# Optimization experiments

Hardware: AMD Instinct MI355X
Metric: run time of the kernel (lower is better)

Reference implementation:

```python
import jax, jax.numpy as jnp
import numpy as np

ALPHA = 5.0  # spatial bandwidth
BETA = 5.0   # feature (bilateral) bandwidth
EPS = 1e-20


def gauss_filter(features, values):
    """Exact dense Gaussian (bilateral) filter: the math the permutohedral
    lattice (pl.apply) approximates.
    features: [B, D, N], values: [B, C, N] -> [B, C, N]
    Q[b,c,i] = sum_j exp(-0.5*||f_i - f_j||^2) * v[b,c,j]
    """
    sq = jnp.sum(features * features, axis=1)  # [B, N]
    d2 = sq[:, :, None] + sq[:, None, :] - 2.0 * jnp.einsum('bdi,bdj->bij', features, features)
    K = jnp.exp(-0.5 * jnp.maximum(d2, 0.0))  # [B, N, N]
    return jnp.einsum('bij,bcj->bci', K, values)


def setup_inputs() -> dict:
    key = jax.random.key(0)
    k1, k2 = jax.random.split(key)
    I = jax.random.normal(k1, (2, 3, 18, 18, 18), dtype=jnp.float32)
    U = jax.random.normal(k2, (2, 4, 18, 18, 18), dtype=jnp.float32)
    return {"I": I, "U": U}


def reference(I, U):
    B, n_feat, X, Y, Z = I.shape
    N = X * Y * Z
    n_ch = U.shape[1]
    # spatial coordinates, scaled by alpha (smoothness kernel part)
    gx, gy, gz = jnp.meshgrid(jnp.arange(X), jnp.arange(Y), jnp.arange(Z), indexing='ij')
    coords = jnp.stack([gx, gy, gz], 0).astype(I.dtype)            # [3, X, Y, Z]
    coords = jnp.broadcast_to(coords[None], (B, 3, X, Y, Z))
    feats = jnp.concatenate([coords / ALPHA, I / BETA], axis=1)    # [B, 3+n_feat, X, Y, Z]
    feats = feats.reshape(B, n_feat + 3, N)
    # normalization: filter an all-ones signal (use_norm=True path)
    ones = jnp.ones((B, 1, N), dtype=I.dtype)
    spatial_norm = 1.0 / jnp.sqrt(gauss_filter(feats, ones) + EPS)  # [B, 1, N]
    # unary -> softmax over channels
    Uf = U.reshape(B, n_ch, N)
    H1 = jax.nn.softmax(Uf, axis=1)                                 # [B, C, N]
    # pairwise message passing (normalized bilateral filter)
    Q1 = gauss_filter(feats, H1 * spatial_norm) * spatial_norm      # [B, C, N]
    # trace(Q1_flat.T @ (1 - H1_flat)) == elementwise sum (same reshape on both)
    loss = jnp.sum(Q1 * (1.0 - H1))
    return loss
```

## Files before the change

kernel.cpp:

```cpp
#include <hip/hip_runtime.h>

#define B_      2
#define NCH     4
#define DIMX    18
#define NPT     (18*18*18)
#define TIL     183
#define ITIL    184
#define NPTP    (ITIL*32)
#define IBLOCKS 23
#define JSP     16
#define NB      (IBLOCKS*JSP*B_)
#define FSC     (1.2011224087864498f / 5.0f)
#define QPAD    -30000.0f

typedef __attribute__((ext_vector_type(8)))  short short8;
typedef __attribute__((ext_vector_type(4)))  short short4_;
typedef __attribute__((ext_vector_type(16))) float f32x16;
typedef __attribute__((ext_vector_type(4)))  int   int4_;

#define EXP2(x) __builtin_amdgcn_exp2f(x)
#define MFMA32(a, b, c) __builtin_amdgcn_mfma_f32_32x32x16_bf16(a, b, c, 0, 0, 0)

__device__ __forceinline__ unsigned short bf16rtn(float f) {
  unsigned u = __float_as_uint(f);
  u += 0x7fffu + ((u >> 16) & 1u);
  return (unsigned short)(u >> 16);
}
__device__ __forceinline__ float bf2f(unsigned short s) {
  return __uint_as_float(((unsigned)s) << 16);
}

__device__ __forceinline__ float blockReduceSum(float v) {
  #pragma unroll
  for (int o = 32; o > 0; o >>= 1) v += __shfl_down(v, o, 64);
  __shared__ float red[4];
  int wid = threadIdx.x >> 6, lane = threadIdx.x & 63;
  if (lane == 0) red[wid] = v;
  __syncthreads();
  v = (threadIdx.x < 4) ? red[threadIdx.x] : 0.0f;
  if (wid == 0) {
    v += __shfl_down(v, 2, 64);
    v += __shfl_down(v, 1, 64);
  }
  return v;
}

__global__ void prep_kernel(const float* __restrict__ I, const float* __restrict__ U,
                            short8* __restrict__ AHI, short8* __restrict__ BHL,
                            float4* __restrict__ H) {
  const short8 zer = {0, 0, 0, 0, 0, 0, 0, 0};
  int idx = blockIdx.x * 256 + threadIdx.x;
  if (idx >= B_ * NPTP) return;
  int bb = idx / NPTP, n = idx - bb * NPTP;
  short8 ahi, bhi, blo;
  float4 hh;
  if (n < NPT) {
    int x = n / (DIMX * DIMX);
    int rem = n - x * DIMX * DIMX;
    int y = rem / DIMX, z = rem - y * DIMX;
    float f0 = x * FSC, f1 = y * FSC, f2 = z * FSC;
    float f3 = I[(size_t)(bb * 3 + 0) * NPT + n] * FSC;
    float f4 = I[(size_t)(bb * 3 + 1) * NPT + n] * FSC;
    float f5 = I[(size_t)(bb * 3 + 2) * NPT + n] * FSC;
    float q = -0.5f * (f0*f0 + f1*f1 + f2*f2 + f3*f3 + f4*f4 + f5*f5);
    float av[8] = {f0, f1, f2, f3, f4, f5, q, 1.0f};
    float bv[8] = {f0, f1, f2, f3, f4, f5, 1.0f, q};
    #pragma unroll
    for (int e = 0; e < 8; ++e) {
      ahi[e] = (short)bf16rtn(av[e]);
      unsigned short bh = bf16rtn(bv[e]);
      bhi[e] = (short)bh;
      blo[e] = (short)bf16rtn(bv[e] - bf2f(bh));
    }
    float u0 = U[(size_t)(bb * NCH + 0) * NPT + n];
    float u1 = U[(size_t)(bb * NCH + 1) * NPT + n];
    float u2 = U[(size_t)(bb * NCH + 2) * NPT + n];
    float u3 = U[(size_t)(bb * NCH + 3) * NPT + n];
    float m = fmaxf(fmaxf(u0, u1), fmaxf(u2, u3));
    float e0 = __expf(u0-m), e1 = __expf(u1-m), e2 = __expf(u2-m), e3 = __expf(u3-m);
    float inv = 1.0f / (e0 + e1 + e2 + e3);
    hh = make_float4(e0*inv, e1*inv, e2*inv, e3*inv);
  } else {
    ahi = zer; bhi = zer; blo = zer;
    bhi[7] = (short)bf16rtn(QPAD);
    hh = make_float4(0.f, 0.f, 0.f, 0.f);
  }
  AHI[idx] = ahi;
  BHL[(size_t)idx * 2]     = bhi;
  BHL[(size_t)idx * 2 + 1] = blo;
  H[idx] = hh;
}

__device__ __forceinline__ float expsum16(const f32x16 acc) {
  float e[16];
  #pragma unroll
  for (int r = 0; r < 16; ++r) e[r] = EXP2(acc[r]);
  float s8[8];
  #pragma unroll
  for (int r = 0; r < 8; ++r) s8[r] = e[2*r] + e[2*r+1];
  float s4[4];
  #pragma unroll
  for (int r = 0; r < 4; ++r) s4[r] = s8[2*r] + s8[2*r+1];
  return (s4[0] + s4[1]) + (s4[2] + s4[3]);
}

__global__ void __launch_bounds__(256) pass1_kernel(const short8* __restrict__ AHI,
                                                    const short8* __restrict__ BHL,
                                                    float* __restrict__ part) {
  const short8 zer = {0, 0, 0, 0, 0, 0, 0, 0};
  int tid = threadIdx.x, wid = tid >> 6, l = tid & 63, h = l >> 5, li = l & 31;
  int bb = blockIdx.z, jc = blockIdx.y;
  int i0 = (blockIdx.x * 8 + wid) * 32 + li;
  int i1 = i0 + 128;
  size_t pbase = (size_t)bb * NPTP;
  int t0 = jc * TIL / JSP, t1 = (jc + 1) * TIL / JSP;

  short8 b1_0 = AHI[pbase + i0];
  short8 b1_1 = AHI[pbase + i1];

  f32x16 z;
  #pragma unroll
  for (int r = 0; r < 16; ++r) z[r] = 0.0f;

  float sacc0 = 0.0f, sacc1 = 0.0f;
  short8 a_cur = BHL[(pbase + (size_t)t0 * 32 + li) * 2 + h];
  for (int t = t0; t < t1; ++t) {
    short8 a_nxt = (t + 1 < t1) ? BHL[(pbase + (size_t)(t+1) * 32 + li) * 2 + h] : zer;
    f32x16 acc0 = MFMA32(a_cur, b1_0, z);
    f32x16 acc1 = MFMA32(a_cur, b1_1, z);
    sacc0 += expsum16(acc0);
    sacc1 += expsum16(acc1);
    a_cur = a_nxt;
  }
  sacc0 += __shfl_xor(sacc0, 32, 64);
  sacc1 += __shfl_xor(sacc1, 32, 64);
  if (h == 0) {
    part[((size_t)bb * JSP + jc) * NPTP + i0] = sacc0;
    part[((size_t)bb * JSP + jc) * NPTP + i1] = sacc1;
  }
}

__global__ void finalize_kernel(const float4* __restrict__ H, const float* __restrict__ part,
                                unsigned short* __restrict__ Vt, float4* __restrict__ G4) {
  int idx = blockIdx.x * 256 + threadIdx.x;
  if (idx >= B_ * NPTP) return;
  int bb = idx / NPTP, ii = idx - bb * NPTP;
  if (ii < NPT) {
    float s = 0.0f;
    #pragma unroll
    for (int k = 0; k < JSP; ++k) s += part[((size_t)bb * JSP + k) * NPTP + ii];
    float nrm = rsqrtf(s + 1e-20f);
    float4 hh = H[idx];
    Vt[((size_t)bb * 4 + 0) * NPTP + ii] = bf16rtn(hh.x * nrm);
    Vt[((size_t)bb * 4 + 1) * NPTP + ii] = bf16rtn(hh.y * nrm);
    Vt[((size_t)bb * 4 + 2) * NPTP + ii] = bf16rtn(hh.z * nrm);
    Vt[((size_t)bb * 4 + 3) * NPTP + ii] = bf16rtn(hh.w * nrm);
    G4[idx] = make_float4((1.0f - hh.x) * nrm, (1.0f - hh.y) * nrm,
                          (1.0f - hh.z) * nrm, (1.0f - hh.w) * nrm);
  } else {
    Vt[((size_t)bb * 4 + 0) * NPTP + ii] = 0;
    Vt[((size_t)bb * 4 + 1) * NPTP + ii] = 0;
    Vt[((size_t)bb * 4 + 2) * NPTP + ii] = 0;
    Vt[((size_t)bb * 4 + 3) * NPTP + ii] = 0;
    G4[idx] = make_float4(0.f, 0.f, 0.f, 0.f);
  }
}

__device__ __forceinline__ void ldv(const unsigned short* __restrict__ vrow, int j32,
                                    int h, bool cok, short8* vf1, short8* vf2) {
  const short4_ zer4 = {0, 0, 0, 0};
  short4_ va = cok ? *(const short4_*)(vrow + j32 + 4*h)      : zer4;
  short4_ vb = cok ? *(const short4_*)(vrow + j32 + 8 + 4*h)  : zer4;
  short4_ vc = cok ? *(const short4_*)(vrow + j32 + 16 + 4*h) : zer4;
  short4_ vd = cok ? *(const short4_*)(vrow + j32 + 24 + 4*h) : zer4;
  short8 f1, f2;
  #pragma unroll
  for (int e = 0; e < 4; ++e) {
    f1[e] = va[e]; f1[4 + e] = vb[e];
    f2[e] = vc[e]; f2[4 + e] = vd[e];
  }
  *vf1 = f1; *vf2 = f2;
}

__device__ __forceinline__ void pv_tile(const f32x16 acc, const short8 vf1,
                                        const short8 vf2, f32x16* d2) {
  float w[16];
  #pragma unroll
  for (int r = 0; r < 16; ++r) w[r] = EXP2(acc[r]);
  int p[8];
  #pragma unroll
  for (int r = 0; r < 8; ++r)
    asm("v_cvt_pk_bf16_f32 %0, %1, %2" : "=v"(p[r]) : "v"(w[2*r]), "v"(w[2*r+1]));
  union { int4_ iv; short8 sv; } u1, u2;
  u1.iv = (int4_){p[0], p[1], p[2], p[3]};
  u2.iv = (int4_){p[4], p[5], p[6], p[7]};
  f32x16 d = *d2;
  d = MFMA32(vf1, u1.sv, d);
  d = MFMA32(vf2, u2.sv, d);
  *d2 = d;
}

__global__ void __launch_bounds__(256) pass2_kernel(const short8* __restrict__ AHI,
                                                    const short8* __restrict__ BHL,
                                                    const unsigned short* __restrict__ Vt,
                                                    const float4* __restrict__ G4,
                                                    float* __restrict__ pl) {
  const short8 zer = {0, 0, 0, 0, 0, 0, 0, 0};
  int tid = threadIdx.x, wid = tid >> 6, l = tid & 63, h = l >> 5, li = l & 31;
  int bb = blockIdx.z, jc = blockIdx.y;
  int i0 = (blockIdx.x * 8 + wid) * 32 + li;
  int i1 = i0 + 128;
  size_t pbase = (size_t)bb * NPTP;
  int t0 = jc * TIL / JSP, t1 = (jc + 1) * TIL / JSP;

  short8 b1_0 = AHI[pbase + i0];
  short8 b1_1 = AHI[pbase + i1];
  float4 g0 = G4[pbase + i0];
  float4 g1 = G4[pbase + i1];
  bool cok = li < 4;
  const unsigned short* vrow = Vt + ((size_t)bb * 4 + (cok ? li : 0)) * NPTP;

  f32x16 z;
  #pragma unroll
  for (int r = 0; r < 16; ++r) z[r] = 0.0f;

  f32x16 d2_0 = z, d2_1 = z;

  short8 a_cur = BHL[(pbase + (size_t)t0 * 32 + li) * 2 + h];
  short8 vf1c, vf2c;
  ldv(vrow, t0 * 32, h, cok, &vf1c, &vf2c);

  for (int t = t0; t < t1; ++t) {
    short8 a_nxt = zer, vf1n = zer, vf2n = zer;
    if (t + 1 < t1) {
      a_nxt = BHL[(pbase + (size_t)(t+1) * 32 + li) * 2 + h];
      ldv(vrow, (t + 1) * 32, h, cok, &vf1n, &vf2n);
    }
    f32x16 acc0 = MFMA32(a_cur, b1_0, z);
    f32x16 acc1 = MFMA32(a_cur, b1_1, z);
    pv_tile(acc0, vf1c, vf2c, &d2_0);
    pv_tile(acc1, vf1c, vf2c, &d2_1);
    a_cur = a_nxt; vf1c = vf1n; vf2c = vf2n;
  }

  float loss = d2_0[0] * g0.x + d2_0[1] * g0.y + d2_0[2] * g0.z + d2_0[3] * g0.w
             + d2_1[0] * g1.x + d2_1[1] * g1.y + d2_1[2] * g1.z + d2_1[3] * g1.w;
  float r = blockReduceSum(loss);
  if (tid == 0) pl[((size_t)bb * JSP + jc) * IBLOCKS + blockIdx.x] = r;
}

__global__ void reduce_kernel(const float* __restrict__ pl, int n, float* __restrict__ out) {
  float v = 0.0f;
  for (int k = threadIdx.x; k < n; k += 256) v += pl[k];
  float r = blockReduceSum(v);
  if (threadIdx.x == 0) out[0] = r;
}

extern "C" void kernel_launch(void* const* d_in, const int* in_sizes, int n_in,
                              void* d_out, int out_size, void* d_ws, size_t ws_size,
                              hipStream_t stream) {
  const float* I = (const float*)d_in[0];
  const float* U = (const float*)d_in[1];
  float* out = (float*)d_out;

  char* w = (char*)d_ws;
  short8* AHI = (short8*)w;                 w += (size_t)B_ * NPTP * 16;
  short8* BHL = (short8*)w;                 w += (size_t)B_ * NPTP * 32;
  float4* H   = (float4*)w;                 w += (size_t)B_ * NPTP * 16;
  float*  part = (float*)w;                 w += (size_t)B_ * JSP * NPTP * 4;
  unsigned short* Vt = (unsigned short*)w;  w += (size_t)B_ * 4 * NPTP * 2;
  float4* G4  = (float4*)w;                 w += (size_t)B_ * NPTP * 16;
  float*  pl  = (float*)w;                  w += (size_t)NB * 4;

  prep_kernel<<<(B_ * NPTP + 255) / 256, 256, 0, stream>>>(I, U, AHI, BHL, H);
  dim3 grid(IBLOCKS, JSP, B_);
  pass1_kernel<<<grid, 256, 0, stream>>>(AHI, BHL, part);
  finalize_kernel<<<(B_ * NPTP + 255) / 256, 256, 0, stream>>>(H, part, Vt, G4);
  pass2_kernel<<<grid, 256, 0, stream>>>(AHI, BHL, Vt, G4, pl);
  reduce_kernel<<<1, 256, 0, stream>>>(pl, NB, out);
}
```

Baseline: 42.45 us.

## Fuse prep, finalize and reduce into two pass kernels with LDS-staged features

Removes the separate prep, finalize and reduce kernels. Each pass block now computes its j-tile features (bf16 hi/lo) and normalized values directly into shared memory, and builds its i-side features on the fly. The final reduction happens in the last-arriving block, using an atomic counter reset by a memset. The j-split rises from 16 to 22 so the grid has more blocks, and launch bounds request 4 blocks per CU. This cuts launch count and global round-trips. The cost is redundant per-block feature, softmax and norm recomputation, and the norm now sums 22 partials instead of 16.

```diff
diff --git a/kernel.cpp b/kernel.cpp
--- a/kernel.cpp
+++ b/kernel.cpp
@@ -8,13 +8,13 @@
 #define ITIL    184
 #define NPTP    (ITIL*32)
 #define IBLOCKS 23
-#define JSP     16
+#define JSP     22
 #define NB      (IBLOCKS*JSP*B_)
+#define MAXT    9
 #define FSC     (1.2011224087864498f / 5.0f)
 #define QPAD    -30000.0f
 
 typedef __attribute__((ext_vector_type(8)))  short short8;
-typedef __attribute__((ext_vector_type(4)))  short short4_;
 typedef __attribute__((ext_vector_type(16))) float f32x16;
 typedef __attribute__((ext_vector_type(4)))  int   int4_;
 
@@ -42,53 +42,62 @@
     v += __shfl_down(v, 2, 64);
     v += __shfl_down(v, 1, 64);
   }
+  __syncthreads();
   return v;
 }
 
-__global__ void prep_kernel(const float* __restrict__ I, const float* __restrict__ U,
-                            short8* __restrict__ AHI, short8* __restrict__ BHL,
-                            float4* __restrict__ H) {
-  const short8 zer = {0, 0, 0, 0, 0, 0, 0, 0};
-  int idx = blockIdx.x * 256 + threadIdx.x;
-  if (idx >= B_ * NPTP) return;
-  int bb = idx / NPTP, n = idx - bb * NPTP;
-  short8 ahi, bhi, blo;
-  float4 hh;
+__device__ __forceinline__ void feat6(const float* __restrict__ I, int bb, int n,
+                                      float f[6], float* q) {
+  int x = n / (DIMX * DIMX);
+  int rem = n - x * DIMX * DIMX;
+  int y = rem / DIMX, zz = rem - y * DIMX;
+  f[0] = x * FSC; f[1] = y * FSC; f[2] = zz * FSC;
+  f[3] = I[(size_t)(bb * 3 + 0) * NPT + n] * FSC;
+  f[4] = I[(size_t)(bb * 3 + 1) * NPT + n] * FSC;
+  f[5] = I[(size_t)(bb * 3 + 2) * NPT + n] * FSC;
+  *q = -0.5f * (f[0]*f[0] + f[1]*f[1] + f[2]*f[2] + f[3]*f[3] + f[4]*f[4] + f[5]*f[5]);
+}
+
+__device__ __forceinline__ void bfeat(const float* __restrict__ I, int bb, int n,
+                                      short8* hi, short8* lo) {
+  short8 h_ = {0,0,0,0,0,0,0,0}, l_ = {0,0,0,0,0,0,0,0};
   if (n < NPT) {
-    int x = n / (DIMX * DIMX);
-    int rem = n - x * DIMX * DIMX;
-    int y = rem / DIMX, z = rem - y * DIMX;
-    float f0 = x * FSC, f1 = y * FSC, f2 = z * FSC;
-    float f3 = I[(size_t)(bb * 3 + 0) * NPT + n] * FSC;
-    float f4 = I[(size_t)(bb * 3 + 1) * NPT + n] * FSC;
-    float f5 = I[(size_t)(bb * 3 + 2) * NPT + n] * FSC;
-    float q = -0.5f * (f0*f0 + f1*f1 + f2*f2 + f3*f3 + f4*f4 + f5*f5);
-    float av[8] = {f0, f1, f2, f3, f4, f5, q, 1.0f};
-    float bv[8] = {f0, f1, f2, f3, f4, f5, 1.0f, q};
+    float f[6], q;
+    feat6(I, bb, n, f, &q);
+    float bv[8] = {f[0], f[1], f[2], f[3], f[4], f[5], 1.0f, q};
     #pragma unroll
     for (int e = 0; e < 8; ++e) {
-      ahi[e] = (short)bf16rtn(av[e]);
       unsigned short bh = bf16rtn(bv[e]);
-      bhi[e] = (short)bh;
-      blo[e] = (short)bf16rtn(bv[e] - bf2f(bh));
-    }
-    float u0 = U[(size_t)(bb * NCH + 0) * NPT + n];
-    float u1 = U[(size_t)(bb * NCH + 1) * NPT + n];
-    float u2 = U[(size_t)(bb * NCH + 2) * NPT + n];
-    float u3 = U[(size_t)(bb * NCH + 3) * NPT + n];
-    float m = fmaxf(fmaxf(u0, u1), fmaxf(u2, u3));
-    float e0 = __expf(u0-m), e1 = __expf(u1-m), e2 = __expf(u2-m), e3 = __expf(u3-m);
-    float inv = 1.0f / (e0 + e1 + e2 + e3);
-    hh = make_float4(e0*inv, e1*inv, e2*inv, e3*inv);
+      h_[e] = (short)bh;
+      l_[e] = (short)bf16rtn(bv[e] - bf2f(bh));
+    }
   } else {
-    ahi = zer; bhi = zer; blo = zer;
-    bhi[7] = (short)bf16rtn(QPAD);
-    hh = make_float4(0.f, 0.f, 0.f, 0.f);
-  }
-  AHI[idx] = ahi;
-  BHL[(size_t)idx * 2]     = bhi;
-  BHL[(size_t)idx * 2 + 1] = blo;
-  H[idx] = hh;
+    h_[7] = (short)bf16rtn(QPAD);
+  }
+  *hi = h_; *lo = l_;
+}
+
+__device__ __forceinline__ short8 afeat(const float* __restrict__ I, int bb, int n) {
+  short8 a = {0,0,0,0,0,0,0,0};
+  if (n < NPT) {
+    float f[6], q;
+    feat6(I, bb, n, f, &q);
+    float av[8] = {f[0], f[1], f[2], f[3], f[4], f[5], q, 1.0f};
+    #pragma unroll
+    for (int e = 0; e < 8; ++e) a[e] = (short)bf16rtn(av[e]);
+  }
+  return a;
+}
+
+__device__ __forceinline__ float4 softmax4(const float* __restrict__ U, int bb, int n) {
+  float u0 = U[(size_t)(bb * NCH + 0) * NPT + n];
+  float u1 = U[(size_t)(bb * NCH + 1) * NPT + n];
+  float u2 = U[(size_t)(bb * NCH + 2) * NPT + n];
+  float u3 = U[(size_t)(bb * NCH + 3) * NPT + n];
+  float m = fmaxf(fmaxf(u0, u1), fmaxf(u2, u3));
+  float e0 = __expf(u0-m), e1 = __expf(u1-m), e2 = __expf(u2-m), e3 = __expf(u3-m);
+  float inv = 1.0f / (e0 + e1 + e2 + e3);
+  return make_float4(e0*inv, e1*inv, e2*inv, e3*inv);
 }
 
 __device__ __forceinline__ float expsum16(const f32x16 acc) {
@@ -104,33 +113,38 @@
   return (s4[0] + s4[1]) + (s4[2] + s4[3]);
 }
 
-__global__ void __launch_bounds__(256) pass1_kernel(const short8* __restrict__ AHI,
-                                                    const short8* __restrict__ BHL,
-                                                    float* __restrict__ part) {
-  const short8 zer = {0, 0, 0, 0, 0, 0, 0, 0};
+__global__ void __launch_bounds__(256, 4) pass1_kernel(const float* __restrict__ I,
+                                                       float* __restrict__ part) {
+  __shared__ short8 bhl[MAXT * 32 * 2];
   int tid = threadIdx.x, wid = tid >> 6, l = tid & 63, h = l >> 5, li = l & 31;
-  int bb = blockIdx.z, jc = blockIdx.y;
-  int i0 = (blockIdx.x * 8 + wid) * 32 + li;
+  int bb = blockIdx.z, jc = blockIdx.y, ib = blockIdx.x;
+  int t0 = jc * TIL / JSP, t1 = (jc + 1) * TIL / JSP;
+  int cnt = (t1 - t0) * 32;
+
+  for (int p = tid; p < cnt; p += 256) {
+    short8 hi, lo;
+    bfeat(I, bb, t0 * 32 + p, &hi, &lo);
+    bhl[p * 2]     = hi;
+    bhl[p * 2 + 1] = lo;
+  }
+
+  int i0 = (ib * 8 + wid) * 32 + li;
   int i1 = i0 + 128;
-  size_t pbase = (size_t)bb * NPTP;
-  int t0 = jc * TIL / JSP, t1 = (jc + 1) * TIL / JSP;
-
-  short8 b1_0 = AHI[pbase + i0];
-  short8 b1_1 = AHI[pbase + i1];
+  short8 b1_0 = afeat(I, bb, i0);
+  short8 b1_1 = afeat(I, bb, i1);
+  __syncthreads();
 
   f32x16 z;
   #pragma unroll
   for (int r = 0; r < 16; ++r) z[r] = 0.0f;
 
   float sacc0 = 0.0f, sacc1 = 0.0f;
-  short8 a_cur = BHL[(pbase + (size_t)t0 * 32 + li) * 2 + h];
   for (int t = t0; t < t1; ++t) {
-    short8 a_nxt = (t + 1 < t1) ? BHL[(pbase + (size_t)(t+1) * 32 + li) * 2 + h] : zer;
-    f32x16 acc0 = MFMA32(a_cur, b1_0, z);
-    f32x16 acc1 = MFMA32(a_cur, b1_1, z);
+    short8 a = bhl[((t - t0) * 32 + li) * 2 + h];
+    f32x16 acc0 = MFMA32(a, b1_0, z);
+    f32x16 acc1 = MFMA32(a, b1_1, z);
     sacc0 += expsum16(acc0);
     sacc1 += expsum16(acc1);
-    a_cur = a_nxt;
   }
   sacc0 += __shfl_xor(sacc0, 32, 64);
   sacc1 += __shfl_xor(sacc1, 32, 64);
@@ -140,120 +154,130 @@
   }
 }
 
-__global__ void finalize_kernel(const float4* __restrict__ H, const float* __restrict__ part,
-                                unsigned short* __restrict__ Vt, float4* __restrict__ G4) {
-  int idx = blockIdx.x * 256 + threadIdx.x;
-  if (idx >= B_ * NPTP) return;
-  int bb = idx / NPTP, ii = idx - bb * NPTP;
-  if (ii < NPT) {
-    float s = 0.0f;
-    #pragma unroll
-    for (int k = 0; k < JSP; ++k) s += part[((size_t)bb * JSP + k) * NPTP + ii];
-    float nrm = rsqrtf(s + 1e-20f);
-    float4 hh = H[idx];
-    Vt[((size_t)bb * 4 + 0) * NPTP + ii] = bf16rtn(hh.x * nrm);
-    Vt[((size_t)bb * 4 + 1) * NPTP + ii] = bf16rtn(hh.y * nrm);
-    Vt[((size_t)bb * 4 + 2) * NPTP + ii] = bf16rtn(hh.z * nrm);
-    Vt[((size_t)bb * 4 + 3) * NPTP + ii] = bf16rtn(hh.w * nrm);
-    G4[idx] = make_float4((1.0f - hh.x) * nrm, (1.0f - hh.y) * nrm,
-                          (1.0f - hh.z) * nrm, (1.0f - hh.w) * nrm);
-  } else {
-    Vt[((size_t)bb * 4 + 0) * NPTP + ii] = 0;
-    Vt[((size_t)bb * 4 + 1) * NPTP + ii] = 0;
-    Vt[((size_t)bb * 4 + 2) * NPTP + ii] = 0;
-    Vt[((size_t)bb * 4 + 3) * NPTP + ii] = 0;
-    G4[idx] = make_float4(0.f, 0.f, 0.f, 0.f);
-  }
-}
-
-__device__ __forceinline__ void ldv(const unsigned short* __restrict__ vrow, int j32,
-                                    int h, bool cok, short8* vf1, short8* vf2) {
-  const short4_ zer4 = {0, 0, 0, 0};
-  short4_ va = cok ? *(const short4_*)(vrow + j32 + 4*h)      : zer4;
-  short4_ vb = cok ? *(const short4_*)(vrow + j32 + 8 + 4*h)  : zer4;
-  short4_ vc = cok ? *(const short4_*)(vrow + j32 + 16 + 4*h) : zer4;
-  short4_ vd = cok ? *(const short4_*)(vrow + j32 + 24 + 4*h) : zer4;
-  short8 f1, f2;
-  #pragma unroll
-  for (int e = 0; e < 4; ++e) {
-    f1[e] = va[e]; f1[4 + e] = vb[e];
-    f2[e] = vc[e]; f2[4 + e] = vd[e];
-  }
-  *vf1 = f1; *vf2 = f2;
-}
-
-__device__ __forceinline__ void pv_tile(const f32x16 acc, const short8 vf1,
-                                        const short8 vf2, f32x16* d2) {
-  float w[16];
-  #pragma unroll
-  for (int r = 0; r < 16; ++r) w[r] = EXP2(acc[r]);
-  int p[8];
-  #pragma unroll
-  for (int r = 0; r < 8; ++r)
-    asm("v_cvt_pk_bf16_f32 %0, %1, %2" : "=v"(p[r]) : "v"(w[2*r]), "v"(w[2*r+1]));
-  union { int4_ iv; short8 sv; } u1, u2;
-  u1.iv = (int4_){p[0], p[1], p[2], p[3]};
-  u2.iv = (int4_){p[4], p[5], p[6], p[7]};
-  f32x16 d = *d2;
-  d = MFMA32(vf1, u1.sv, d);
-  d = MFMA32(vf2, u2.sv, d);
-  *d2 = d;
-}
-
-__global__ void __launch_bounds__(256) pass2_kernel(const short8* __restrict__ AHI,
-                                                    const short8* __restrict__ BHL,
-                                                    const unsigned short* __restrict__ Vt,
-                                                    const float4* __restrict__ G4,
-                                                    float* __restrict__ pl) {
+__global__ void __launch_bounds__(256, 4) pass2_kernel(const float* __restrict__ I,
+                                                       const float* __restrict__ U,
+                                                       const float* __restrict__ part,
+                                                       float* __restrict__ pl,
+                                                       unsigned* __restrict__ cnt_,
+                                                       float* __restrict__ out) {
+  __shared__ short8 bhl[MAXT * 32 * 2];
+  __shared__ short8 vt8[MAXT * 4 * 4];
+  __shared__ bool isLast;
+  int tid = threadIdx.x, wid = tid >> 6, l = tid & 63, h = l >> 5, li = l & 31;
+  int bb = blockIdx.z, jc = blockIdx.y, ib = blockIdx.x;
+  int t0 = jc * TIL / JSP, t1 = (jc + 1) * TIL / JSP;
+  int cnt = (t1 - t0) * 32;
+  unsigned short* vtp = (unsigned short*)vt8;
+
+  for (int p = tid; p < cnt; p += 256) {
+    int j = t0 * 32 + p;
+    short8 hi, lo;
+    bfeat(I, bb, j, &hi, &lo);
+    bhl[p * 2]     = hi;
+    bhl[p * 2 + 1] = lo;
+    float4 hv = make_float4(0.f, 0.f, 0.f, 0.f);
+    float nrm = 0.0f;
+    if (j < NPT) {
+      float s = 0.0f;
+      #pragma unroll
+      for (int k = 0; k < JSP; ++k) s += part[((size_t)bb * JSP + k) * NPTP + j];
+      nrm = rsqrtf(s + 1e-20f);
+      hv = softmax4(U, bb, j);
+    }
+    int tt = p >> 5, jj = p & 31;
+    int g1 = jj >> 4, r = jj & 15;
+    int slot = (g1 * 2 + ((r >> 2) & 1)) * 8 + (r & 3) + 4 * (r >> 3);
+    vtp[(tt * 4 + 0) * 32 + slot] = bf16rtn(hv.x * nrm);
+    vtp[(tt * 4 + 1) * 32 + slot] = bf16rtn(hv.y * nrm);
+    vtp[(tt * 4 + 2) * 32 + slot] = bf16rtn(hv.z * nrm);
+    vtp[(tt * 4 + 3) * 32 + slot] = bf16rtn(hv.w * nrm);
+  }
+
+  int i0 = (ib * 8 + wid) * 32 + li;
+  int i1 = i0 + 128;
+  short8 b1_0 = afeat(I, bb, i0);
+  short8 b1_1 = afeat(I, bb, i1);
+  float4 g0 = make_float4(0.f, 0.f, 0.f, 0.f), g1v = g0;
+  {
+    if (i0 < NPT) {
+      float s = 0.0f;
+      #pragma unroll
+      for (int k = 0; k < JSP; ++k) s += part[((size_t)bb * JSP + k) * NPTP + i0];
+      float nrm = rsqrtf(s + 1e-20f);
+      float4 hh = softmax4(U, bb, i0);
+      g0 = make_float4((1.f-hh.x)*nrm, (1.f-hh.y)*nrm, (1.f-hh.z)*nrm, (1.f-hh.w)*nrm);
+    }
+    if (i1 < NPT) {
+      float s = 0.0f;
+      #pragma unroll
+      for (int k = 0; k < JSP; ++k) s += part[((size_t)bb * JSP + k) * NPTP + i1];
+      float nrm = rsqrtf(s + 1e-20f);
+      float4 hh = softmax4(U, bb, i1);
+      g1v = make_float4((1.f-hh.x)*nrm, (1.f-hh.y)*nrm, (1.f-hh.z)*nrm, (1.f-hh.w)*nrm);
+    }
+  }
+  __syncthreads();
+
   const short8 zer = {0, 0, 0, 0, 0, 0, 0, 0};
-  int tid = threadIdx.x, wid = tid >> 6, l = tid & 63, h = l >> 5, li = l & 31;
-  int bb = blockIdx.z, jc = blockIdx.y;
-  int i0 = (blockIdx.x * 8 + wid) * 32 + li;
-  int i1 = i0 + 128;
-  size_t pbase = (size_t)bb * NPTP;
-  int t0 = jc * TIL / JSP, t1 = (jc + 1) * TIL / JSP;
-
-  short8 b1_0 = AHI[pbase + i0];
-  short8 b1_1 = AHI[pbase + i1];
-  float4 g0 = G4[pbase + i0];
-  float4 g1 = G4[pbase + i1];
   bool cok = li < 4;
-  const unsigned short* vrow = Vt + ((size_t)bb * 4 + (cok ? li : 0)) * NPTP;
+  int cc = cok ? li : 0;
 
   f32x16 z;
   #pragma unroll
   for (int r = 0; r < 16; ++r) z[r] = 0.0f;
-
   f32x16 d2_0 = z, d2_1 = z;
 
-  short8 a_cur = BHL[(pbase + (size_t)t0 * 32 + li) * 2 + h];
-  short8 vf1c, vf2c;
-  ldv(vrow, t0 * 32, h, cok, &vf1c, &vf2c);
-
   for (int t = t0; t < t1; ++t) {
-    short8 a_nxt = zer, vf1n = zer, vf2n = zer;
-    if (t + 1 < t1) {
-      a_nxt = BHL[(pbase + (size_t)(t+1) * 32 + li) * 2 + h];
-      ldv(vrow, (t + 1) * 32, h, cok, &vf1n, &vf2n);
-    }
-    f32x16 acc0 = MFMA32(a_cur, b1_0, z);
-    f32x16 acc1 = MFMA32(a_cur, b1_1, z);
-    pv_tile(acc0, vf1c, vf2c, &d2_0);
-    pv_tile(acc1, vf1c, vf2c, &d2_1);
-    a_cur = a_nxt; vf1c = vf1n; vf2c = vf2n;
+    int tt = t - t0;
+    short8 a = bhl[(tt * 32 + li) * 2 + h];
+    short8 vf1 = vt8[(tt * 4 + cc) * 4 + h];
+    short8 vf2 = vt8[(tt * 4 + cc) * 4 + 2 + h];
+    vf1 = cok ? vf1 : zer;
+    vf2 = cok ? vf2 : zer;
+
+    f32x16 acc0 = MFMA32(a, b1_0, z);
+    f32x16 acc1 = MFMA32(a, b1_1, z);
+
+    float w0[16], w1[16];
+    #pragma unroll
+    for (int r = 0; r < 16; ++r) { w0[r] = EXP2(acc0[r]); w1[r] = EXP2(acc1[r]); }
+    int p0[8], p1[8];
+    #pragma unroll
+    for (int r = 0; r < 8; ++r) {
+      asm("v_cvt_pk_bf16_f32 %0, %1, %2" : "=v"(p0[r]) : "v"(w0[2*r]), "v"(w0[2*r+1]));
+      asm("v_cvt_pk_bf16_f32 %0, %1, %2" : "=v"(p1[r]) : "v"(w1[2*r]), "v"(w1[2*r+1]));
+    }
+    union { int4_ iv; short8 sv; } u1a, u2a, u1b, u2b;
+    u1a.iv = (int4_){p0[0], p0[1], p0[2], p0[3]};
+    u2a.iv = (int4_){p0[4], p0[5], p0[6], p0[7]};
+    u1b.iv = (int4_){p1[0], p1[1], p1[2], p1[3]};
+    u2b.iv = (int4_){p1[4], p1[5], p1[6], p1[7]};
+
+    d2_0 = MFMA32(vf1, u1a.sv, d2_0);
+    d2_0 = MFMA32(vf2, u2a.sv, d2_0);
+    d2_1 = MFMA32(vf1, u1b.sv, d2_1);
+    d2_1 = MFMA32(vf2, u2b.sv, d2_1);
   }
 
   float loss = d2_0[0] * g0.x + d2_0[1] * g0.y + d2_0[2] * g0.z + d2_0[3] * g0.w
-             + d2_1[0] * g1.x + d2_1[1] * g1.y + d2_1[2] * g1.z + d2_1[3] * g1.w;
+             + d2_1[0] * g1v.x + d2_1[1] * g1v.y + d2_1[2] * g1v.z + d2_1[3] * g1v.w;
   float r = blockReduceSum(loss);
-  if (tid == 0) pl[((size_t)bb * JSP + jc) * IBLOCKS + blockIdx.x] = r;
-}
-
-__global__ void reduce_kernel(const float* __restrict__ pl, int n, float* __restrict__ out) {
-  float v = 0.0f;
-  for (int k = threadIdx.x; k < n; k += 256) v += pl[k];
-  float r = blockReduceSum(v);
-  if (threadIdx.x == 0) out[0] = r;
+
+  int blkflat = ((bb * JSP + jc) * IBLOCKS + ib);
+  if (tid == 0) {
+    pl[blkflat] = r;
+    __threadfence();
+    unsigned prev = atomicAdd(cnt_, 1u);
+    isLast = (prev == NB - 1);
+  }
+  __syncthreads();
+  if (isLast) {
+    __threadfence();
+    float v = 0.0f;
+    for (int k = tid; k < NB; k += 256) v += pl[k];
+    float rr = blockReduceSum(v);
+    if (tid == 0) out[0] = rr;
+  }
 }
 
 extern "C" void kernel_launch(void* const* d_in, const int* in_sizes, int n_in,
@@ -264,18 +288,12 @@
   float* out = (float*)d_out;
 
   char* w = (char*)d_ws;
-  short8* AHI = (short8*)w;                 w += (size_t)B_ * NPTP * 16;
-  short8* BHL = (short8*)w;                 w += (size_t)B_ * NPTP * 32;
-  float4* H   = (float4*)w;                 w += (size_t)B_ * NPTP * 16;
-  float*  part = (float*)w;                 w += (size_t)B_ * JSP * NPTP * 4;
-  unsigned short* Vt = (unsigned short*)w;  w += (size_t)B_ * 4 * NPTP * 2;
-  float4* G4  = (float4*)w;                 w += (size_t)B_ * NPTP * 16;
-  float*  pl  = (float*)w;                  w += (size_t)NB * 4;
-
-  prep_kernel<<<(B_ * NPTP + 255) / 256, 256, 0, stream>>>(I, U, AHI, BHL, H);
+  float* part = (float*)w;          w += (size_t)B_ * JSP * NPTP * 4;
+  float* pl   = (float*)w;          w += (size_t)NB * 4;
+  unsigned* cnt_ = (unsigned*)w;    w += 64;
+
+  hipMemsetAsync(cnt_, 0, 4, stream);
   dim3 grid(IBLOCKS, JSP, B_);
-  pass1_kernel<<<grid, 256, 0, stream>>>(AHI, BHL, part);
-  finalize_kernel<<<(B_ * NPTP + 255) / 256, 256, 0, stream>>>(H, part, Vt, G4);
-  pass2_kernel<<<grid, 256, 0, stream>>>(AHI, BHL, Vt, G4, pl);
-  reduce_kernel<<<1, 256, 0, stream>>>(pl, NB, out);
-}
+  pass1_kernel<<<grid, 256, 0, stream>>>(I, part);
+  pass2_kernel<<<grid, 256, 0, stream>>>(I, U, part, pl, cnt_, out);
+}
```

Result: slower. 48.34 us (+13.9%).

## Fuse final reduction into pass2 via last-block atomic counter and widen j-split

Applied to the files above, without the earlier changes.

Drops the separate reduce kernel launch: each pass2 block writes its partial and bumps an atomic counter, and the last block sums all partials and writes the output. A memset of the counter is added per call. JSP goes from 16 to 22, giving more blocks for better CU occupancy but more partials (and a larger pass1 part buffer). The two exp/MFMA tiles are also interleaved in one inline body to expose ILP.

```diff
diff --git a/kernel.cpp b/kernel.cpp
--- a/kernel.cpp
+++ b/kernel.cpp
@@ -8,7 +8,7 @@
 #define ITIL    184
 #define NPTP    (ITIL*32)
 #define IBLOCKS 23
-#define JSP     16
+#define JSP     22
 #define NB      (IBLOCKS*JSP*B_)
 #define FSC     (1.2011224087864498f / 5.0f)
 #define QPAD    -30000.0f
@@ -42,6 +42,7 @@
     v += __shfl_down(v, 2, 64);
     v += __shfl_down(v, 1, 64);
   }
+  __syncthreads();
   return v;
 }
 
@@ -182,30 +183,15 @@
   *vf1 = f1; *vf2 = f2;
 }
 
-__device__ __forceinline__ void pv_tile(const f32x16 acc, const short8 vf1,
-                                        const short8 vf2, f32x16* d2) {
-  float w[16];
-  #pragma unroll
-  for (int r = 0; r < 16; ++r) w[r] = EXP2(acc[r]);
-  int p[8];
-  #pragma unroll
-  for (int r = 0; r < 8; ++r)
-    asm("v_cvt_pk_bf16_f32 %0, %1, %2" : "=v"(p[r]) : "v"(w[2*r]), "v"(w[2*r+1]));
-  union { int4_ iv; short8 sv; } u1, u2;
-  u1.iv = (int4_){p[0], p[1], p[2], p[3]};
-  u2.iv = (int4_){p[4], p[5], p[6], p[7]};
-  f32x16 d = *d2;
-  d = MFMA32(vf1, u1.sv, d);
-  d = MFMA32(vf2, u2.sv, d);
-  *d2 = d;
-}
-
 __global__ void __launch_bounds__(256) pass2_kernel(const short8* __restrict__ AHI,
                                                     const short8* __restrict__ BHL,
                                                     const unsigned short* __restrict__ Vt,
                                                     const float4* __restrict__ G4,
-                                                    float* __restrict__ pl) {
+                                                    float* __restrict__ pl,
+                                                    unsigned* __restrict__ cnt_,
+                                                    float* __restrict__ out) {
   const short8 zer = {0, 0, 0, 0, 0, 0, 0, 0};
+  __shared__ bool isLast;
   int tid = threadIdx.x, wid = tid >> 6, l = tid & 63, h = l >> 5, li = l & 31;
   int bb = blockIdx.z, jc = blockIdx.y;
   int i0 = (blockIdx.x * 8 + wid) * 32 + li;
@@ -216,14 +202,13 @@
   short8 b1_0 = AHI[pbase + i0];
   short8 b1_1 = AHI[pbase + i1];
   float4 g0 = G4[pbase + i0];
-  float4 g1 = G4[pbase + i1];
+  float4 g1v = G4[pbase + i1];
   bool cok = li < 4;
   const unsigned short* vrow = Vt + ((size_t)bb * 4 + (cok ? li : 0)) * NPTP;
 
   f32x16 z;
   #pragma unroll
   for (int r = 0; r < 16; ++r) z[r] = 0.0f;
-
   f32x16 d2_0 = z, d2_1 = z;
 
   short8 a_cur = BHL[(pbase + (size_t)t0 * 32 + li) * 2 + h];
@@ -238,22 +223,49 @@
     }
     f32x16 acc0 = MFMA32(a_cur, b1_0, z);
     f32x16 acc1 = MFMA32(a_cur, b1_1, z);
-    pv_tile(acc0, vf1c, vf2c, &d2_0);
-    pv_tile(acc1, vf1c, vf2c, &d2_1);
+
+    float w0[16], w1[16];
+    #pragma unroll
+    for (int r = 0; r < 16; ++r) { w0[r] = EXP2(acc0[r]); w1[r] = EXP2(acc1[r]); }
+    int p0[8], p1[8];
+    #pragma unroll
+    for (int r = 0; r < 8; ++r) {
+      asm("v_cvt_pk_bf16_f32 %0, %1, %2" : "=v"(p0[r]) : "v"(w0[2*r]), "v"(w0[2*r+1]));
+      asm("v_cvt_pk_bf16_f32 %0, %1, %2" : "=v"(p1[r]) : "v"(w1[2*r]), "v"(w1[2*r+1]));
+    }
+    union { int4_ iv; short8 sv; } u1a, u2a, u1b, u2b;
+    u1a.iv = (int4_){p0[0], p0[1], p0[2], p0[3]};
+    u2a.iv = (int4_){p0[4], p0[5], p0[6], p0[7]};
+    u1b.iv = (int4_){p1[0], p1[1], p1[2], p1[3]};
+    u2b.iv = (int4_){p1[4], p1[5], p1[6], p1[7]};
+
+    d2_0 = MFMA32(vf1c, u1a.sv, d2_0);
+    d2_0 = MFMA32(vf2c, u2a.sv, d2_0);
+    d2_1 = MFMA32(vf1c, u1b.sv, d2_1);
+    d2_1 = MFMA32(vf2c, u2b.sv, d2_1);
+
     a_cur = a_nxt; vf1c = vf1n; vf2c = vf2n;
   }
 
   float loss = d2_0[0] * g0.x + d2_0[1] * g0.y + d2_0[2] * g0.z + d2_0[3] * g0.w
-             + d2_1[0] * g1.x + d2_1[1] * g1.y + d2_1[2] * g1.z + d2_1[3] * g1.w;
+             + d2_1[0] * g1v.x + d2_1[1] * g1v.y + d2_1[2] * g1v.z + d2_1[3] * g1v.w;
   float r = blockReduceSum(loss);
-  if (tid == 0) pl[((size_t)bb * JSP + jc) * IBLOCKS + blockIdx.x] = r;
-}
-
-__global__ void reduce_kernel(const float* __restrict__ pl, int n, float* __restrict__ out) {
-  float v = 0.0f;
-  for (int k = threadIdx.x; k < n; k += 256) v += pl[k];
-  float r = blockReduceSum(v);
-  if (threadIdx.x == 0) out[0] = r;
+
+  int blkflat = ((bb * JSP + jc) * IBLOCKS + blockIdx.x);
+  if (tid == 0) {
+    pl[blkflat] = r;
+    __threadfence();
+    unsigned prev = atomicAdd(cnt_, 1u);
+    isLast = (prev == NB - 1);
+  }
+  __syncthreads();
+  if (isLast) {
+    __threadfence();
+    float v = 0.0f;
+    for (int k = tid; k < NB; k += 256) v += pl[k];
+    float rr = blockReduceSum(v);
+    if (tid == 0) out[0] = rr;
+  }
 }
 
 extern "C" void kernel_launch(void* const* d_in, const int* in_sizes, int n_in,
@@ -271,11 +283,12 @@
   unsigned short* Vt = (unsigned short*)w;  w += (size_t)B_ * 4 * NPTP * 2;
   float4* G4  = (float4*)w;                 w += (size_t)B_ * NPTP * 16;
   float*  pl  = (float*)w;                  w += (size_t)NB * 4;
-
+  unsigned* cnt_ = (unsigned*)w;            w += 64;
+
+  hipMemsetAsync(cnt_, 0, 4, stream);
   prep_kernel<<<(B_ * NPTP + 255) / 256, 256, 0, stream>>>(I, U, AHI, BHL, H);
   dim3 grid(IBLOCKS, JSP, B_);
   pass1_kernel<<<grid, 256, 0, stream>>>(AHI, BHL, part);
   finalize_kernel<<<(B_ * NPTP + 255) / 256, 256, 0, stream>>>(H, part, Vt, G4);
-  pass2_kernel<<<grid, 256, 0, stream>>>(AHI, BHL, Vt, G4, pl);
-  reduce_kernel<<<1, 256, 0, stream>>>(pl, NB, out);
-}
+  pass2_kernel<<<grid, 256, 0, stream>>>(AHI, BHL, Vt, G4, pl, cnt_, out);
+}
```

After: 57.37 us. 35.1% more time.
